# Performance work log

Hardware: AMD Instinct MI355X
Metric: run time of the kernel (lower is better)

## Reference

```python
import jax, jax.numpy as jnp
import numpy as np

D = 1024
HS = 64
NH = D // HS
NEG_INF = -1e30


def setup_inputs() -> dict:
    key = jax.random.key(0)
    ks = jax.random.split(key, 8)
    B, S = 4, 2048
    x = jax.random.normal(ks[0], (B, S, D), dtype=jnp.float32)
    y = jax.random.normal(ks[1], (B, S, D), dtype=jnp.float32)
    pad_mask = jnp.ones((B, S), dtype=jnp.int32)
    time_attention = jnp.ones((S, S), dtype=jnp.int32)
    scale = 1.0 / np.sqrt(D)
    Wq = jax.random.normal(ks[2], (D, D), dtype=jnp.float32) * scale
    Wk = jax.random.normal(ks[3], (D, D), dtype=jnp.float32) * scale
    Wv = jax.random.normal(ks[4], (D, D), dtype=jnp.float32) * scale
    Wp = jax.random.normal(ks[5], (D, D), dtype=jnp.float32) * scale
    bp = jnp.zeros((D,), dtype=jnp.float32)
    return {"x": x, "y": y, "pad_mask": pad_mask, "time_attention": time_attention,
            "Wq": Wq, "Wk": Wk, "Wv": Wv, "Wp": Wp, "bp": bp}


def reference(x, y, pad_mask, time_attention, Wq, Wk, Wv, Wp, bp):
    B, S, _ = x.shape
    Sy = y.shape[1]
    # q/k/v projections (Linear: x @ W.T), split into heads -> [B, H, S, hs]
    q = (y @ Wq.T).reshape(B, Sy, NH, HS).transpose(0, 2, 1, 3)
    k = (x @ Wk.T).reshape(B, S, NH, HS).transpose(0, 2, 1, 3)
    v = (x @ Wv.T).reshape(B, S, NH, HS).transpose(0, 2, 1, 3)
    # scaled scores [B, H, Sy, S]
    att = jnp.einsum('bhqe,bhke->bhqk', q, k) * (HS ** -0.5)
    # causal mask (tril[:S, :S])
    causal = jnp.tril(jnp.ones((S, S), dtype=jnp.bool_))
    att = jnp.where(causal[None, None, :Sy, :], att, NEG_INF)
    # pad mask over kv positions
    att = jnp.where(pad_mask[:, None, None, :] != 0, att, NEG_INF)
    # time attention mask [Sq, Sk]
    att = jnp.where(time_attention[None, None, :Sy, :] != 0, att, NEG_INF)
    p = jax.nn.softmax(att, axis=-1)  # dropout p=0 -> identity
    out = jnp.einsum('bhqk,bhke->bhqe', p, v)
    out = out.transpose(0, 2, 1, 3).reshape(B, Sy, D)
    return out @ Wp.T + bp
```

## Files before the change

kernel.cpp:

```cpp
#include <hip/hip_runtime.h>
#include <hip/hip_bf16.h>
#include <stdint.h>
#include <stddef.h>


typedef __attribute__((ext_vector_type(4))) float f32x4;
typedef __attribute__((ext_vector_type(8))) short s16x8;
typedef __attribute__((ext_vector_type(4))) float float4v;
typedef __attribute__((ext_vector_type(4))) int i32x4;
typedef __attribute__((ext_vector_type(2))) unsigned int u32x2;

#define DEV __device__ __forceinline__

constexpr int Bsz = 4, Sseq = 2048, Dm = 1024, NHn = 16, HSn = 64;
constexpr float QSCALE = 0.125f * 1.4426950408889634f;

constexpr size_t SZ_BF_XY = (size_t)Bsz * Sseq * Dm * 2;
constexpr size_t SZ_W     = (size_t)Dm * Dm * 2;
constexpr size_t OFF_XBF  = 0;
constexpr size_t OFF_YBF  = OFF_XBF + SZ_BF_XY;
constexpr size_t OFF_WQ   = OFF_YBF + SZ_BF_XY;
constexpr size_t OFF_WK   = OFF_WQ + SZ_W;
constexpr size_t OFF_WV   = OFF_WK + SZ_W;
constexpr size_t OFF_WP   = OFF_WV + SZ_W;
constexpr size_t OFF_QWS  = OFF_WP + SZ_W;
constexpr size_t OFF_KWS  = OFF_QWS + SZ_BF_XY;
constexpr size_t OFF_VTWS = OFF_KWS + SZ_BF_XY;
constexpr size_t OFF_OWS  = OFF_VTWS + SZ_BF_XY;
constexpr size_t OFF_FLAG = OFF_OWS + SZ_BF_XY;

DEV unsigned short f2bf(float f) {
  union { float f; unsigned int u; } v; v.f = f;
  unsigned int r = (v.u + 0x7FFFu + ((v.u >> 16) & 1u)) >> 16;
  return (unsigned short)r;
}

DEV void gll16(const void* g, void* l) {
  __builtin_amdgcn_global_load_lds((const __attribute__((address_space(1))) unsigned int*)g,
                                   (__attribute__((address_space(3))) unsigned int*)l, 16, 0, 0);
}

DEV unsigned int cvtpk(float a, float b) {
  unsigned int r;
  asm("v_cvt_pk_bf16_f32 %0, %1, %2" : "=v"(r) : "v"(a), "v"(b));
  return r;
}

union U8 { s16x8 v; unsigned int u[4]; };

__global__ void cvt_all(const float* __restrict__ x, const float* __restrict__ y,
                        const float* __restrict__ Wq, const float* __restrict__ Wk,
                        const float* __restrict__ Wv, const float* __restrict__ Wp,
                        const int* __restrict__ pad, const int* __restrict__ tmask,
                        char* __restrict__ ws, int* __restrict__ flags) {
  const int blk = blockIdx.x;
  if (blk >= 10240) {
    int bad = 0;
    if (blk < 10248) {
      const i32x4 v = ((const i32x4*)pad)[(blk - 10240) * 256 + threadIdx.x];
      bad = (v[0] == 0) | (v[1] == 0) | (v[2] == 0) | (v[3] == 0);
    } else {
      const i32x4* tp = (const i32x4*)tmask + ((size_t)(blk - 10248) * 256 + threadIdx.x) * 2;
      i32x4 v0 = tp[0], v1 = tp[1];
      bad = (v0[0] == 0) | (v0[1] == 0) | (v0[2] == 0) | (v0[3] == 0) |
            (v1[0] == 0) | (v1[1] == 0) | (v1[2] == 0) | (v1[3] == 0);
    }
    if (__builtin_amdgcn_ballot_w64(bad) != 0 && (threadIdx.x & 63) == 0)
      atomicOr(flags, 1);
    return;
  }
  const float* src;
  unsigned short* dst;
  int b8;
  float scale = 1.f;
  if (blk < 4096)      { src = x;  dst = (unsigned short*)(ws + OFF_XBF); b8 = blk; }
  else if (blk < 8192) { src = y;  dst = (unsigned short*)(ws + OFF_YBF); b8 = blk - 4096; }
  else if (blk < 8704) { src = Wq; dst = (unsigned short*)(ws + OFF_WQ);  b8 = blk - 8192; scale = QSCALE; }
  else if (blk < 9216) { src = Wk; dst = (unsigned short*)(ws + OFF_WK);  b8 = blk - 8704; }
  else if (blk < 9728) { src = Wv; dst = (unsigned short*)(ws + OFF_WV);  b8 = blk - 9216; }
  else                 { src = Wp; dst = (unsigned short*)(ws + OFF_WP);  b8 = blk - 9728; }
  const size_t i = (size_t)b8 * 256 + threadIdx.x;
  const float4v* s = (const float4v*)src + i * 2;
  float4v a = s[0], b = s[1];
  s16x8 o;
  o[0] = (short)f2bf(a[0] * scale); o[1] = (short)f2bf(a[1] * scale);
  o[2] = (short)f2bf(a[2] * scale); o[3] = (short)f2bf(a[3] * scale);
  o[4] = (short)f2bf(b[0] * scale); o[5] = (short)f2bf(b[1] * scale);
  o[6] = (short)f2bf(b[2] * scale); o[7] = (short)f2bf(b[3] * scale);
  *(s16x8*)(dst + i * 8) = o;
}

__global__ __launch_bounds__(256) void q_gemm(const unsigned short* __restrict__ A,
                                              const unsigned short* __restrict__ W,
                                              unsigned short* __restrict__ outb) {
  constexpr int K = 1024;
  __shared__ unsigned short sm[2][8192];
  const int tid = threadIdx.x;
  const int w = tid >> 6, lane = tid & 63, lo = lane & 15, hi = lane >> 4;
  const int wm = w >> 1, wn = w & 1;
  const int m0 = blockIdx.x * 128, n0 = blockIdx.y * 128;
  f32x4 acc[4][4] = {};

  auto stage = [&](int buf, int k0) {
#pragma unroll
    for (int h = 0; h < 2; ++h) {
      int c = w * 64 + h * 256 + lane;
      gll16(A + (size_t)(m0 + (c >> 2)) * K + k0 + (c & 3) * 8, &sm[buf][0] + (size_t)(w * 64 + h * 256) * 8);
      gll16(W + (size_t)(n0 + (c >> 2)) * K + k0 + (c & 3) * 8, &sm[buf][4096] + (size_t)(w * 64 + h * 256) * 8);
    }
  };

  stage(0, 0);
  __syncthreads();
  for (int t = 0; t < 32; ++t) {
    if (t < 31) stage((t + 1) & 1, (t + 1) * 32);
    const unsigned short* lA = &sm[t & 1][0];
    const unsigned short* lB = &sm[t & 1][4096];
    s16x8 af[4], bfr[4];
#pragma unroll
    for (int mi = 0; mi < 4; ++mi) af[mi] = *(const s16x8*)&lA[(wm * 64 + mi * 16 + lo) * 32 + hi * 8];
#pragma unroll
    for (int ni = 0; ni < 4; ++ni) bfr[ni] = *(const s16x8*)&lB[(wn * 64 + ni * 16 + lo) * 32 + hi * 8];
#pragma unroll
    for (int mi = 0; mi < 4; ++mi)
#pragma unroll
      for (int ni = 0; ni < 4; ++ni)
        acc[mi][ni] = __builtin_amdgcn_mfma_f32_16x16x32_bf16(af[mi], bfr[ni], acc[mi][ni], 0, 0, 0);
    __syncthreads();
  }
#pragma unroll
  for (int mi = 0; mi < 4; ++mi)
#pragma unroll
    for (int ni = 0; ni < 4; ++ni)
#pragma unroll
      for (int j = 0; j < 4; ++j) {
        int m = m0 + wm * 64 + mi * 16 + hi * 4 + j;
        int n = n0 + wn * 64 + ni * 16 + lo;
        int b = m >> 11, s = m & 2047, hh = n >> 6, e = n & 63;
        outb[((size_t)(b * NHn + hh) * Sseq + s) * HSn + e] = f2bf(acc[mi][ni][j]);
      }
}

__global__ __launch_bounds__(256, 2) void kv_gemm(const unsigned short* __restrict__ A,
                                                  const unsigned short* __restrict__ Wk,
                                                  const unsigned short* __restrict__ Wv,
                                                  unsigned short* __restrict__ kws,
                                                  unsigned short* __restrict__ vtw) {
  constexpr int K = 1024;
  __shared__ unsigned short sm[2][12288];
  const int tid = threadIdx.x;
  const int w = tid >> 6, lane = tid & 63, lo = lane & 15, hi = lane >> 4;
  const int wm = w >> 1, wn = w & 1;
  const int m0 = blockIdx.x * 128, n0 = blockIdx.y * 128;
  f32x4 acck[4][4] = {}, accv[4][4] = {};

  auto stage = [&](int buf, int k0) {
#pragma unroll
    for (int h = 0; h < 2; ++h) {
      int c = w * 64 + h * 256 + lane;
      size_t roff = (size_t)(c >> 2) * K + k0 + (c & 3) * 8;
      size_t loff = (size_t)(w * 64 + h * 256) * 8;
      gll16(A + (size_t)m0 * K + roff, &sm[buf][0] + loff);
      gll16(Wk + (size_t)n0 * K + roff, &sm[buf][4096] + loff);
      gll16(Wv + (size_t)n0 * K + roff, &sm[buf][8192] + loff);
    }
  };

  stage(0, 0);
  __syncthreads();
  for (int t = 0; t < 32; ++t) {
    if (t < 31) stage((t + 1) & 1, (t + 1) * 32);
    const unsigned short* lA = &sm[t & 1][0];
    const unsigned short* lBk = &sm[t & 1][4096];
    const unsigned short* lBv = &sm[t & 1][8192];
    s16x8 af[4], bfk[4], bfv[4];
#pragma unroll
    for (int mi = 0; mi < 4; ++mi) af[mi] = *(const s16x8*)&lA[(wm * 64 + mi * 16 + lo) * 32 + hi * 8];
#pragma unroll
    for (int ni = 0; ni < 4; ++ni) {
      bfk[ni] = *(const s16x8*)&lBk[(wn * 64 + ni * 16 + lo) * 32 + hi * 8];
      bfv[ni] = *(const s16x8*)&lBv[(wn * 64 + ni * 16 + lo) * 32 + hi * 8];
    }
#pragma unroll
    for (int mi = 0; mi < 4; ++mi)
#pragma unroll
      for (int ni = 0; ni < 4; ++ni) {
        acck[mi][ni] = __builtin_amdgcn_mfma_f32_16x16x32_bf16(af[mi], bfk[ni], acck[mi][ni], 0, 0, 0);
        accv[mi][ni] = __builtin_amdgcn_mfma_f32_16x16x32_bf16(af[mi], bfv[ni], accv[mi][ni], 0, 0, 0);
      }
    __syncthreads();
  }

#pragma unroll
  for (int mi = 0; mi < 4; ++mi)
#pragma unroll
    for (int ni = 0; ni < 4; ++ni)
#pragma unroll
      for (int j = 0; j < 4; ++j) {
        int m = m0 + wm * 64 + mi * 16 + hi * 4 + j;
        int n = n0 + wn * 64 + ni * 16 + lo;
        int b = m >> 11, s = m & 2047, hh = n >> 6, e = n & 63;
        kws[((size_t)(b * NHn + hh) * Sseq + s) * HSn + e] = f2bf(acck[mi][ni][j]);
      }
  unsigned short* tp = &sm[0][0];
  __syncthreads();
#pragma unroll
  for (int mi = 0; mi < 4; ++mi)
#pragma unroll
    for (int ni = 0; ni < 4; ++ni)
#pragma unroll
      for (int j = 0; j < 4; ++j) {
        int ml = wm * 64 + mi * 16 + hi * 4 + j;
        int nl = wn * 64 + ni * 16 + lo;
        tp[(size_t)nl * 136 + ml] = f2bf(accv[mi][ni][j]);
      }
  __syncthreads();
  int nl = tid >> 1, half = tid & 1;
  int b = m0 >> 11, hh = (n0 + nl) >> 6, e = (n0 + nl) & 63;
  unsigned short* dst = vtw + ((size_t)(b * NHn + hh) * HSn + e) * Sseq + (m0 & 2047) + half * 64;
#pragma unroll
  for (int i = 0; i < 8; ++i)
    *(s16x8*)(dst + i * 8) = *(const s16x8*)&tp[(size_t)nl * 136 + half * 64 + i * 8];
}

__global__ __launch_bounds__(256) void gemm_p(const unsigned short* __restrict__ A,
                                              const unsigned short* __restrict__ W,
                                              float* __restrict__ outf,
                                              const float* __restrict__ bias) {
  constexpr int K = 1024;
  __shared__ unsigned short sm[2][8192];
  const int tid = threadIdx.x;
  const int w = tid >> 6, lane = tid & 63, lo = lane & 15, hi = lane >> 4;
  const int wm = w >> 1, wn = w & 1;
  const int m0 = blockIdx.x * 128, n0 = blockIdx.y * 128;
  f32x4 acc[4][4] = {};

  auto stage = [&](int buf, int k0) {
#pragma unroll
    for (int h = 0; h < 2; ++h) {
      int c = w * 64 + h * 256 + lane;
      gll16(A + (size_t)(m0 + (c >> 2)) * K + k0 + (c & 3) * 8, &sm[buf][0] + (size_t)(w * 64 + h * 256) * 8);
      gll16(W + (size_t)(n0 + (c >> 2)) * K + k0 + (c & 3) * 8, &sm[buf][4096] + (size_t)(w * 64 + h * 256) * 8);
    }
  };

  stage(0, 0);
  __syncthreads();
  for (int t = 0; t < 32; ++t) {
    if (t < 31) stage((t + 1) & 1, (t + 1) * 32);
    const unsigned short* lA = &sm[t & 1][0];
    const unsigned short* lB = &sm[t & 1][4096];
    s16x8 af[4], bfr[4];
#pragma unroll
    for (int mi = 0; mi < 4; ++mi) af[mi] = *(const s16x8*)&lA[(wm * 64 + mi * 16 + lo) * 32 + hi * 8];
#pragma unroll
    for (int ni = 0; ni < 4; ++ni) bfr[ni] = *(const s16x8*)&lB[(wn * 64 + ni * 16 + lo) * 32 + hi * 8];
#pragma unroll
    for (int mi = 0; mi < 4; ++mi)
#pragma unroll
      for (int ni = 0; ni < 4; ++ni)
        acc[mi][ni] = __builtin_amdgcn_mfma_f32_16x16x32_bf16(af[mi], bfr[ni], acc[mi][ni], 0, 0, 0);
    __syncthreads();
  }
  float bv[4];
#pragma unroll
  for (int ni = 0; ni < 4; ++ni) bv[ni] = bias[n0 + wn * 64 + ni * 16 + lo];
#pragma unroll
  for (int mi = 0; mi < 4; ++mi)
#pragma unroll
    for (int ni = 0; ni < 4; ++ni)
#pragma unroll
      for (int j = 0; j < 4; ++j) {
        int m = m0 + wm * 64 + mi * 16 + hi * 4 + j;
        int n = n0 + wn * 64 + ni * 16 + lo;
        outf[(size_t)m * 1024 + n] = acc[mi][ni][j] + bv[ni];
      }
}

DEV void attn_unit16(const unsigned short* __restrict__ kbc,
                     const unsigned short* __restrict__ vbc,
                     const s16x8 (&qf)[2], f32x4 (&oacc)[4], f32x4& lacc,
                     float& mrun, const s16x8& ones,
                     int k0, int qw0, int lo, int hi, int b,
                     const int* __restrict__ pad, const int* __restrict__ tmask,
                     bool trivial) {
  if (k0 > qw0 + 15) return;

  f32x4 st[4];
  __builtin_amdgcn_s_setprio(1);
#pragma unroll
  for (int t = 0; t < 4; ++t) {
    f32x4 z = {0.f, 0.f, 0.f, 0.f};
#pragma unroll
    for (int kk = 0; kk < 2; ++kk) {
      s16x8 kfr = *(const s16x8*)&kbc[(t * 16 + lo) * 72 + kk * 32 + hi * 8];
      z = __builtin_amdgcn_mfma_f32_16x16x32_bf16(kfr, qf[kk], z, 0, 0, 0);
    }
    st[t] = z;
  }
  __builtin_amdgcn_s_setprio(0);
  const int qg = qw0 + lo;
  const int kgb = k0 + hi * 8;
  if (k0 + 63 > qw0) {
#pragma unroll
    for (int t = 0; t < 4; ++t)
#pragma unroll
      for (int j = 0; j < 4; ++j) {
        int kg = kgb + ((t & 1) << 5) + ((t >> 1) << 2) + j;
        if (kg > qg) st[t][j] = -3e38f;
      }
  }
  if (!trivial) {
#pragma unroll
    for (int t = 0; t < 4; ++t)
#pragma unroll
      for (int j = 0; j < 4; ++j) {
        int kg = kgb + ((t & 1) << 5) + ((t >> 1) << 2) + j;
        if (!pad[b * Sseq + kg] || !tmask[(size_t)qg * Sseq + kg]) st[t][j] = -3e38f;
      }
  }
  float m0v = fmaxf(fmaxf(st[0][0], st[0][1]), fmaxf(st[0][2], st[0][3]));
  float m1v = fmaxf(fmaxf(st[1][0], st[1][1]), fmaxf(st[1][2], st[1][3]));
  float m2v = fmaxf(fmaxf(st[2][0], st[2][1]), fmaxf(st[2][2], st[2][3]));
  float m3v = fmaxf(fmaxf(st[3][0], st[3][1]), fmaxf(st[3][2], st[3][3]));
  float mx = fmaxf(fmaxf(m0v, m1v), fmaxf(m2v, m3v));
  mx = fmaxf(mx, __shfl_xor(mx, 16, 64));
  mx = fmaxf(mx, __shfl_xor(mx, 32, 64));
  if (!__all(mx <= mrun + 11.f)) {
    const float mnew = fmaxf(mrun, mx);
    const float al = __builtin_amdgcn_exp2f(mrun - mnew);
    mrun = mnew;
#pragma unroll
    for (int et = 0; et < 4; ++et) oacc[et] *= al;
    lacc *= al;
  }
  unsigned int pk[4][2];
#pragma unroll
  for (int t = 0; t < 4; ++t) {
    float p0 = __builtin_amdgcn_exp2f(st[t][0] - mrun);
    float p1 = __builtin_amdgcn_exp2f(st[t][1] - mrun);
    float p2 = __builtin_amdgcn_exp2f(st[t][2] - mrun);
    float p3 = __builtin_amdgcn_exp2f(st[t][3] - mrun);
    pk[t][0] = cvtpk(p0, p1);
    pk[t][1] = cvtpk(p2, p3);
  }
  U8 pf0, pf1;
  pf0.u[0] = pk[0][0]; pf0.u[1] = pk[0][1]; pf0.u[2] = pk[2][0]; pf0.u[3] = pk[2][1];
  pf1.u[0] = pk[1][0]; pf1.u[1] = pk[1][1]; pf1.u[2] = pk[3][0]; pf1.u[3] = pk[3][1];
  __builtin_amdgcn_s_setprio(1);
#pragma unroll
  for (int et = 0; et < 4; ++et) {
    s16x8 vf0 = *(const s16x8*)&vbc[(et * 16 + lo) * 72 + hi * 8];
    s16x8 vf1 = *(const s16x8*)&vbc[(et * 16 + lo) * 72 + 32 + hi * 8];
    oacc[et] = __builtin_amdgcn_mfma_f32_16x16x32_bf16(vf0, pf0.v, oacc[et], 0, 0, 0);
    oacc[et] = __builtin_amdgcn_mfma_f32_16x16x32_bf16(vf1, pf1.v, oacc[et], 0, 0, 0);
  }
  lacc = __builtin_amdgcn_mfma_f32_16x16x32_bf16(ones, pf0.v, lacc, 0, 0, 0);
  lacc = __builtin_amdgcn_mfma_f32_16x16x32_bf16(ones, pf1.v, lacc, 0, 0, 0);
  __builtin_amdgcn_s_setprio(0);
}

DEV void attn_epi16(f32x4 (&oacc)[4], float lrun,
                    unsigned short* __restrict__ scr,
                    unsigned short* __restrict__ O, int b, int hh, int qw0,
                    int lane, int lo, int hi) {
  const float inv = 1.f / lrun;
#pragma unroll
  for (int et = 0; et < 4; ++et) {
    f32x4 o = oacc[et] * inv;
    u32x2 d = {cvtpk(o[0], o[1]), cvtpk(o[2], o[3])};
    *(u32x2*)&scr[lo * 72 + et * 16 + hi * 4] = d;
  }
  int q = lane >> 2, seg = lane & 3;
  unsigned short* dst = O + ((size_t)b * Sseq + qw0 + q) * Dm + hh * HSn + seg * 16;
  *(s16x8*)dst = *(const s16x8*)&scr[q * 72 + seg * 16];
  *(s16x8*)(dst + 8) = *(const s16x8*)&scr[q * 72 + seg * 16 + 8];
}

__global__ __launch_bounds__(512, 4) void attn_kernel(const unsigned short* __restrict__ Q,
                                                      const unsigned short* __restrict__ Kg,
                                                      const unsigned short* __restrict__ Vt,
                                                      unsigned short* __restrict__ O,
                                                      const int* __restrict__ pad,
                                                      const int* __restrict__ tmask,
                                                      const int* __restrict__ flags) {
  __shared__ unsigned short kb[2][64 * 72];
  __shared__ unsigned short vb[2][64 * 72];

  const int ip = blockIdx.y, bh = blockIdx.x;
  const int b = bh >> 4, hh = bh & 15;
  const int tid = threadIdx.x, w = tid >> 6, lane = tid & 63, lo = lane & 15, hi = lane >> 4;
  const int qtA = ip, qtB = 15 - ip;
  const int qw0A = qtA * 128 + w * 16, qw0B = qtB * 128 + w * 16;
  const int ktA = 2 * qtA + 1;
  const int ktmax = 2 * qtB + 2;
  const bool trivial = flags[0] == 0;

  const unsigned short* Qb = Q + (size_t)bh * Sseq * HSn;
  const unsigned short* Kb = Kg + (size_t)bh * Sseq * HSn;
  const unsigned short* Vb = Vt + (size_t)bh * HSn * Sseq;

  s16x8 qfA[2], qfB[2];
#pragma unroll
  for (int kk = 0; kk < 2; ++kk) {
    qfA[kk] = *(const s16x8*)&Qb[(size_t)(qw0A + lo) * HSn + kk * 32 + hi * 8];
    qfB[kk] = *(const s16x8*)&Qb[(size_t)(qw0B + lo) * HSn + kk * 32 + hi * 8];
  }

  s16x8 ones;
#pragma unroll
  for (int j = 0; j < 8; ++j) ones[j] = (short)0x3F80;

  f32x4 oaccA[4] = {}, oaccB[4] = {};
  f32x4 laccA = {}, laccB = {};
  float mrunA = -3e38f, mrunB = -3e38f;

  const int shalf = tid >> 8, st_t = tid & 255;
  const int sr = st_t >> 2, sc = (st_t & 3) * 16;
  const int srK = ((sr & 0x1C) << 1) | ((sr & 0x20) >> 3) | (sr & 3);

  s16x8 r0, r1;
  if (shalf == 0) {
    const unsigned short* gk = Kb + (size_t)srK * HSn + sc;
    r0 = *(const s16x8*)gk; r1 = *(const s16x8*)(gk + 8);
    *(s16x8*)&kb[0][sr * 72 + sc] = r0; *(s16x8*)&kb[0][sr * 72 + sc + 8] = r1;
  } else {
    const unsigned short* gv = Vb + (size_t)sr * Sseq + sc;
    r0 = *(const s16x8*)gv; r1 = *(const s16x8*)(gv + 8);
    *(s16x8*)&vb[0][sr * 72 + sc] = r0; *(s16x8*)&vb[0][sr * 72 + sc + 8] = r1;
  }
  __syncthreads();

  for (int kt = 0; kt < ktmax; ++kt) {
    const int cur = kt & 1, k0 = kt * 64;
    const bool pre = (kt + 1 < ktmax);
    if (pre) {
      const int k1 = k0 + 64;
      if (shalf == 0) {
        const unsigned short* gk = Kb + (size_t)(k1 + srK) * HSn + sc;
        r0 = *(const s16x8*)gk; r1 = *(const s16x8*)(gk + 8);
      } else {
        const unsigned short* gv = Vb + (size_t)sr * Sseq + k1 + sc;
        r0 = *(const s16x8*)gv; r1 = *(const s16x8*)(gv + 8);
      }
    }
    const unsigned short* kbc = kb[cur];
    const unsigned short* vbc = vb[cur];
    if (kt <= ktA)
      attn_unit16(kbc, vbc, qfA, oaccA, laccA, mrunA, ones,
                  k0, qw0A, lo, hi, b, pad, tmask, trivial);
    attn_unit16(kbc, vbc, qfB, oaccB, laccB, mrunB, ones,
                k0, qw0B, lo, hi, b, pad, tmask, trivial);
    if (pre) {
      const int nb = cur ^ 1;
      if (shalf == 0) {
        *(s16x8*)&kb[nb][sr * 72 + sc] = r0; *(s16x8*)&kb[nb][sr * 72 + sc + 8] = r1;
      } else {
        *(s16x8*)&vb[nb][sr * 72 + sc] = r0; *(s16x8*)&vb[nb][sr * 72 + sc + 8] = r1;
      }
    }
    __syncthreads();
  }

  unsigned short* scr = (unsigned short*)kb + (size_t)w * 1152;
  attn_epi16(oaccA, laccA[0], scr, O, b, hh, qw0A, lane, lo, hi);
  attn_epi16(oaccB, laccB[0], scr, O, b, hh, qw0B, lane, lo, hi);
}

extern "C" void kernel_launch(void* const* d_in, const int* in_sizes, int n_in,
                              void* d_out, int out_size, void* d_ws, size_t ws_size,
                              hipStream_t stream) {
  const float* x = (const float*)d_in[0];
  const float* y = (const float*)d_in[1];
  const int* pad = (const int*)d_in[2];
  const int* tmask = (const int*)d_in[3];
  const float* Wq = (const float*)d_in[4];
  const float* Wk = (const float*)d_in[5];
  const float* Wv = (const float*)d_in[6];
  const float* Wp = (const float*)d_in[7];
  const float* bp = (const float*)d_in[8];

  char* ws = (char*)d_ws;
  unsigned short* xbf = (unsigned short*)(ws + OFF_XBF);
  unsigned short* ybf = (unsigned short*)(ws + OFF_YBF);
  unsigned short* wqb = (unsigned short*)(ws + OFF_WQ);
  unsigned short* wkb = (unsigned short*)(ws + OFF_WK);
  unsigned short* wvb = (unsigned short*)(ws + OFF_WV);
  unsigned short* wpb = (unsigned short*)(ws + OFF_WP);
  unsigned short* qws = (unsigned short*)(ws + OFF_QWS);
  unsigned short* kws = (unsigned short*)(ws + OFF_KWS);
  unsigned short* vtw = (unsigned short*)(ws + OFF_VTWS);
  unsigned short* ows = (unsigned short*)(ws + OFF_OWS);
  int* flags = (int*)(ws + OFF_FLAG);

  hipMemsetAsync(flags, 0, 4, stream);
  cvt_all<<<12296, 256, 0, stream>>>(x, y, Wq, Wk, Wv, Wp, pad, tmask, ws, flags);

  q_gemm<<<dim3(64, 8), 256, 0, stream>>>(ybf, wqb, qws);
  kv_gemm<<<dim3(64, 8), 256, 0, stream>>>(xbf, wkb, wvb, kws, vtw);

  attn_kernel<<<dim3(64, 8), 512, 0, stream>>>(qws, kws, vtw, ows, pad, tmask, flags);

  gemm_p<<<dim3(64, 8), 256, 0, stream>>>(ows, wpb, (float*)d_out, bp);
}
```

Before: 183.6 us.

## Give each attention wave 32 query rows to reuse K/V fragments

The attention block shrinks from 8 waves to 4, and each wave now handles two 16-row query sub-tiles. Each K and V fragment read from LDS feeds two MFMAs instead of one, which halves LDS traffic per FLOP. Each thread now stages both K and V for the next tile, and the epilogue writes 32 rows per wave. The cost is higher register pressure (launch bounds 256,2) and fewer waves per block to hide latency.

Result: no change. 186.0 us (+1.3%).

```diff
diff --git a/kernel.cpp b/kernel.cpp
--- a/kernel.cpp
+++ b/kernel.cpp
@@ -277,107 +277,124 @@
       }
 }
 
-DEV void attn_unit16(const unsigned short* __restrict__ kbc,
+DEV void attn_unit32(const unsigned short* __restrict__ kbc,
                      const unsigned short* __restrict__ vbc,
-                     const s16x8 (&qf)[2], f32x4 (&oacc)[4], f32x4& lacc,
-                     float& mrun, const s16x8& ones,
+                     const s16x8 (&qf)[2][2], f32x4 (&oacc)[4][2], f32x4 (&lacc)[2],
+                     float (&mrun)[2], const s16x8& ones,
                      int k0, int qw0, int lo, int hi, int b,
                      const int* __restrict__ pad, const int* __restrict__ tmask,
                      bool trivial) {
-  if (k0 > qw0 + 15) return;
-
-  f32x4 st[4];
+  if (k0 > qw0 + 31) return;
+
+  f32x4 st[2][4];
   __builtin_amdgcn_s_setprio(1);
 #pragma unroll
   for (int t = 0; t < 4; ++t) {
-    f32x4 z = {0.f, 0.f, 0.f, 0.f};
-#pragma unroll
-    for (int kk = 0; kk < 2; ++kk) {
-      s16x8 kfr = *(const s16x8*)&kbc[(t * 16 + lo) * 72 + kk * 32 + hi * 8];
-      z = __builtin_amdgcn_mfma_f32_16x16x32_bf16(kfr, qf[kk], z, 0, 0, 0);
-    }
-    st[t] = z;
+    const s16x8 kf0 = *(const s16x8*)&kbc[(t * 16 + lo) * 72 + hi * 8];
+    const s16x8 kf1 = *(const s16x8*)&kbc[(t * 16 + lo) * 72 + 32 + hi * 8];
+    f32x4 z0 = {0.f, 0.f, 0.f, 0.f}, z1 = {0.f, 0.f, 0.f, 0.f};
+    z0 = __builtin_amdgcn_mfma_f32_16x16x32_bf16(kf0, qf[0][0], z0, 0, 0, 0);
+    z0 = __builtin_amdgcn_mfma_f32_16x16x32_bf16(kf1, qf[0][1], z0, 0, 0, 0);
+    z1 = __builtin_amdgcn_mfma_f32_16x16x32_bf16(kf0, qf[1][0], z1, 0, 0, 0);
+    z1 = __builtin_amdgcn_mfma_f32_16x16x32_bf16(kf1, qf[1][1], z1, 0, 0, 0);
+    st[0][t] = z0; st[1][t] = z1;
   }
   __builtin_amdgcn_s_setprio(0);
-  const int qg = qw0 + lo;
+
   const int kgb = k0 + hi * 8;
-  if (k0 + 63 > qw0) {
-#pragma unroll
-    for (int t = 0; t < 4; ++t)
-#pragma unroll
-      for (int j = 0; j < 4; ++j) {
-        int kg = kgb + ((t & 1) << 5) + ((t >> 1) << 2) + j;
-        if (kg > qg) st[t][j] = -3e38f;
-      }
-  }
-  if (!trivial) {
-#pragma unroll
-    for (int t = 0; t < 4; ++t)
-#pragma unroll
-      for (int j = 0; j < 4; ++j) {
-        int kg = kgb + ((t & 1) << 5) + ((t >> 1) << 2) + j;
-        if (!pad[b * Sseq + kg] || !tmask[(size_t)qg * Sseq + kg]) st[t][j] = -3e38f;
-      }
-  }
-  float m0v = fmaxf(fmaxf(st[0][0], st[0][1]), fmaxf(st[0][2], st[0][3]));
-  float m1v = fmaxf(fmaxf(st[1][0], st[1][1]), fmaxf(st[1][2], st[1][3]));
-  float m2v = fmaxf(fmaxf(st[2][0], st[2][1]), fmaxf(st[2][2], st[2][3]));
-  float m3v = fmaxf(fmaxf(st[3][0], st[3][1]), fmaxf(st[3][2], st[3][3]));
-  float mx = fmaxf(fmaxf(m0v, m1v), fmaxf(m2v, m3v));
-  mx = fmaxf(mx, __shfl_xor(mx, 16, 64));
-  mx = fmaxf(mx, __shfl_xor(mx, 32, 64));
-  if (!__all(mx <= mrun + 11.f)) {
-    const float mnew = fmaxf(mrun, mx);
-    const float al = __builtin_amdgcn_exp2f(mrun - mnew);
-    mrun = mnew;
-#pragma unroll
-    for (int et = 0; et < 4; ++et) oacc[et] *= al;
-    lacc *= al;
-  }
-  unsigned int pk[4][2];
-#pragma unroll
-  for (int t = 0; t < 4; ++t) {
-    float p0 = __builtin_amdgcn_exp2f(st[t][0] - mrun);
-    float p1 = __builtin_amdgcn_exp2f(st[t][1] - mrun);
-    float p2 = __builtin_amdgcn_exp2f(st[t][2] - mrun);
-    float p3 = __builtin_amdgcn_exp2f(st[t][3] - mrun);
-    pk[t][0] = cvtpk(p0, p1);
-    pk[t][1] = cvtpk(p2, p3);
-  }
-  U8 pf0, pf1;
-  pf0.u[0] = pk[0][0]; pf0.u[1] = pk[0][1]; pf0.u[2] = pk[2][0]; pf0.u[3] = pk[2][1];
-  pf1.u[0] = pk[1][0]; pf1.u[1] = pk[1][1]; pf1.u[2] = pk[3][0]; pf1.u[3] = pk[3][1];
+  U8 pf[2][2];
+#pragma unroll
+  for (int mq = 0; mq < 2; ++mq) {
+    const int qg = qw0 + mq * 16 + lo;
+    if (k0 + 63 > qw0) {
+#pragma unroll
+      for (int t = 0; t < 4; ++t)
+#pragma unroll
+        for (int j = 0; j < 4; ++j) {
+          int kg = kgb + ((t & 1) << 5) + ((t >> 1) << 2) + j;
+          if (kg > qg) st[mq][t][j] = -3e38f;
+        }
+    }
+    if (!trivial) {
+#pragma unroll
+      for (int t = 0; t < 4; ++t)
+#pragma unroll
+        for (int j = 0; j < 4; ++j) {
+          int kg = kgb + ((t & 1) << 5) + ((t >> 1) << 2) + j;
+          if (!pad[b * Sseq + kg] || !tmask[(size_t)qg * Sseq + kg]) st[mq][t][j] = -3e38f;
+        }
+    }
+    float m0v = fmaxf(fmaxf(st[mq][0][0], st[mq][0][1]), fmaxf(st[mq][0][2], st[mq][0][3]));
+    float m1v = fmaxf(fmaxf(st[mq][1][0], st[mq][1][1]), fmaxf(st[mq][1][2], st[mq][1][3]));
+    float m2v = fmaxf(fmaxf(st[mq][2][0], st[mq][2][1]), fmaxf(st[mq][2][2], st[mq][2][3]));
+    float m3v = fmaxf(fmaxf(st[mq][3][0], st[mq][3][1]), fmaxf(st[mq][3][2], st[mq][3][3]));
+    float mx = fmaxf(fmaxf(m0v, m1v), fmaxf(m2v, m3v));
+    mx = fmaxf(mx, __shfl_xor(mx, 16, 64));
+    mx = fmaxf(mx, __shfl_xor(mx, 32, 64));
+    if (!__all(mx <= mrun[mq] + 11.f)) {
+      const float mnew = fmaxf(mrun[mq], mx);
+      const float al = __builtin_amdgcn_exp2f(mrun[mq] - mnew);
+      mrun[mq] = mnew;
+#pragma unroll
+      for (int et = 0; et < 4; ++et) oacc[et][mq] *= al;
+      lacc[mq] *= al;
+    }
+    unsigned int pk[4][2];
+#pragma unroll
+    for (int t = 0; t < 4; ++t) {
+      float p0 = __builtin_amdgcn_exp2f(st[mq][t][0] - mrun[mq]);
+      float p1 = __builtin_amdgcn_exp2f(st[mq][t][1] - mrun[mq]);
+      float p2 = __builtin_amdgcn_exp2f(st[mq][t][2] - mrun[mq]);
+      float p3 = __builtin_amdgcn_exp2f(st[mq][t][3] - mrun[mq]);
+      pk[t][0] = cvtpk(p0, p1);
+      pk[t][1] = cvtpk(p2, p3);
+    }
+    pf[mq][0].u[0] = pk[0][0]; pf[mq][0].u[1] = pk[0][1];
+    pf[mq][0].u[2] = pk[2][0]; pf[mq][0].u[3] = pk[2][1];
+    pf[mq][1].u[0] = pk[1][0]; pf[mq][1].u[1] = pk[1][1];
+    pf[mq][1].u[2] = pk[3][0]; pf[mq][1].u[3] = pk[3][1];
+  }
+
   __builtin_amdgcn_s_setprio(1);
 #pragma unroll
   for (int et = 0; et < 4; ++et) {
-    s16x8 vf0 = *(const s16x8*)&vbc[(et * 16 + lo) * 72 + hi * 8];
-    s16x8 vf1 = *(const s16x8*)&vbc[(et * 16 + lo) * 72 + 32 + hi * 8];
-    oacc[et] = __builtin_amdgcn_mfma_f32_16x16x32_bf16(vf0, pf0.v, oacc[et], 0, 0, 0);
-    oacc[et] = __builtin_amdgcn_mfma_f32_16x16x32_bf16(vf1, pf1.v, oacc[et], 0, 0, 0);
-  }
-  lacc = __builtin_amdgcn_mfma_f32_16x16x32_bf16(ones, pf0.v, lacc, 0, 0, 0);
-  lacc = __builtin_amdgcn_mfma_f32_16x16x32_bf16(ones, pf1.v, lacc, 0, 0, 0);
+    const s16x8 vf0 = *(const s16x8*)&vbc[(et * 16 + lo) * 72 + hi * 8];
+    const s16x8 vf1 = *(const s16x8*)&vbc[(et * 16 + lo) * 72 + 32 + hi * 8];
+    oacc[et][0] = __builtin_amdgcn_mfma_f32_16x16x32_bf16(vf0, pf[0][0].v, oacc[et][0], 0, 0, 0);
+    oacc[et][0] = __builtin_amdgcn_mfma_f32_16x16x32_bf16(vf1, pf[0][1].v, oacc[et][0], 0, 0, 0);
+    oacc[et][1] = __builtin_amdgcn_mfma_f32_16x16x32_bf16(vf0, pf[1][0].v, oacc[et][1], 0, 0, 0);
+    oacc[et][1] = __builtin_amdgcn_mfma_f32_16x16x32_bf16(vf1, pf[1][1].v, oacc[et][1], 0, 0, 0);
+  }
+  lacc[0] = __builtin_amdgcn_mfma_f32_16x16x32_bf16(ones, pf[0][0].v, lacc[0], 0, 0, 0);
+  lacc[0] = __builtin_amdgcn_mfma_f32_16x16x32_bf16(ones, pf[0][1].v, lacc[0], 0, 0, 0);
+  lacc[1] = __builtin_amdgcn_mfma_f32_16x16x32_bf16(ones, pf[1][0].v, lacc[1], 0, 0, 0);
+  lacc[1] = __builtin_amdgcn_mfma_f32_16x16x32_bf16(ones, pf[1][1].v, lacc[1], 0, 0, 0);
   __builtin_amdgcn_s_setprio(0);
 }
 
-DEV void attn_epi16(f32x4 (&oacc)[4], float lrun,
+DEV void attn_epi32(f32x4 (&oacc)[4][2], f32x4 (&lacc)[2],
                     unsigned short* __restrict__ scr,
                     unsigned short* __restrict__ O, int b, int hh, int qw0,
                     int lane, int lo, int hi) {
-  const float inv = 1.f / lrun;
+  const float inv0 = 1.f / lacc[0][0];
+  const float inv1 = 1.f / lacc[1][0];
 #pragma unroll
   for (int et = 0; et < 4; ++et) {
-    f32x4 o = oacc[et] * inv;
-    u32x2 d = {cvtpk(o[0], o[1]), cvtpk(o[2], o[3])};
-    *(u32x2*)&scr[lo * 72 + et * 16 + hi * 4] = d;
-  }
-  int q = lane >> 2, seg = lane & 3;
-  unsigned short* dst = O + ((size_t)b * Sseq + qw0 + q) * Dm + hh * HSn + seg * 16;
-  *(s16x8*)dst = *(const s16x8*)&scr[q * 72 + seg * 16];
-  *(s16x8*)(dst + 8) = *(const s16x8*)&scr[q * 72 + seg * 16 + 8];
-}
-
-__global__ __launch_bounds__(512, 4) void attn_kernel(const unsigned short* __restrict__ Q,
+    f32x4 o0 = oacc[et][0] * inv0;
+    f32x4 o1 = oacc[et][1] * inv1;
+    u32x2 d0 = {cvtpk(o0[0], o0[1]), cvtpk(o0[2], o0[3])};
+    u32x2 d1 = {cvtpk(o1[0], o1[1]), cvtpk(o1[2], o1[3])};
+    *(u32x2*)&scr[(0 * 16 + lo) * 72 + et * 16 + hi * 4] = d0;
+    *(u32x2*)&scr[(1 * 16 + lo) * 72 + et * 16 + hi * 4] = d1;
+  }
+  int q = lane & 31, half = lane >> 5;
+  unsigned short* dst = O + ((size_t)b * Sseq + qw0 + q) * Dm + hh * HSn + half * 32;
+#pragma unroll
+  for (int i = 0; i < 4; ++i)
+    *(s16x8*)(dst + i * 8) = *(const s16x8*)&scr[q * 72 + half * 32 + i * 8];
+}
+
+__global__ __launch_bounds__(256, 2) void attn_kernel(const unsigned short* __restrict__ Q,
                                                       const unsigned short* __restrict__ Kg,
                                                       const unsigned short* __restrict__ Vt,
                                                       unsigned short* __restrict__ O,
@@ -391,7 +408,7 @@
   const int b = bh >> 4, hh = bh & 15;
   const int tid = threadIdx.x, w = tid >> 6, lane = tid & 63, lo = lane & 15, hi = lane >> 4;
   const int qtA = ip, qtB = 15 - ip;
-  const int qw0A = qtA * 128 + w * 16, qw0B = qtB * 128 + w * 16;
+  const int qw0A = qtA * 128 + w * 32, qw0B = qtB * 128 + w * 32;
   const int ktA = 2 * qtA + 1;
   const int ktmax = 2 * qtB + 2;
   const bool trivial = flags[0] == 0;
@@ -400,35 +417,35 @@
   const unsigned short* Kb = Kg + (size_t)bh * Sseq * HSn;
   const unsigned short* Vb = Vt + (size_t)bh * HSn * Sseq;
 
-  s16x8 qfA[2], qfB[2];
-#pragma unroll
-  for (int kk = 0; kk < 2; ++kk) {
-    qfA[kk] = *(const s16x8*)&Qb[(size_t)(qw0A + lo) * HSn + kk * 32 + hi * 8];
-    qfB[kk] = *(const s16x8*)&Qb[(size_t)(qw0B + lo) * HSn + kk * 32 + hi * 8];
-  }
+  s16x8 qfA[2][2], qfB[2][2];
+#pragma unroll
+  for (int mq = 0; mq < 2; ++mq)
+#pragma unroll
+    for (int kk = 0; kk < 2; ++kk) {
+      qfA[mq][kk] = *(const s16x8*)&Qb[(size_t)(qw0A + mq * 16 + lo) * HSn + kk * 32 + hi * 8];
+      qfB[mq][kk] = *(const s16x8*)&Qb[(size_t)(qw0B + mq * 16 + lo) * HSn + kk * 32 + hi * 8];
+    }
 
   s16x8 ones;
 #pragma unroll
   for (int j = 0; j < 8; ++j) ones[j] = (short)0x3F80;
 
-  f32x4 oaccA[4] = {}, oaccB[4] = {};
-  f32x4 laccA = {}, laccB = {};
-  float mrunA = -3e38f, mrunB = -3e38f;
-
-  const int shalf = tid >> 8, st_t = tid & 255;
-  const int sr = st_t >> 2, sc = (st_t & 3) * 16;
+  f32x4 oaccA[4][2] = {}, oaccB[4][2] = {};
+  f32x4 laccA[2] = {}, laccB[2] = {};
+  float mrunA[2] = {-3e38f, -3e38f}, mrunB[2] = {-3e38f, -3e38f};
+
+  const int sr = tid >> 2, sc = (tid & 3) * 16;
   const int srK = ((sr & 0x1C) << 1) | ((sr & 0x20) >> 3) | (sr & 3);
 
-  s16x8 r0, r1;
-  if (shalf == 0) {
+  s16x8 rk0, rk1, rv0, rv1;
+  {
     const unsigned short* gk = Kb + (size_t)srK * HSn + sc;
-    r0 = *(const s16x8*)gk; r1 = *(const s16x8*)(gk + 8);
-    *(s16x8*)&kb[0][sr * 72 + sc] = r0; *(s16x8*)&kb[0][sr * 72 + sc + 8] = r1;
-  } else {
+    rk0 = *(const s16x8*)gk; rk1 = *(const s16x8*)(gk + 8);
     const unsigned short* gv = Vb + (size_t)sr * Sseq + sc;
-    r0 = *(const s16x8*)gv; r1 = *(const s16x8*)(gv + 8);
-    *(s16x8*)&vb[0][sr * 72 + sc] = r0; *(s16x8*)&vb[0][sr * 72 + sc + 8] = r1;
-  }
+    rv0 = *(const s16x8*)gv; rv1 = *(const s16x8*)(gv + 8);
+  }
+  *(s16x8*)&kb[0][sr * 72 + sc] = rk0; *(s16x8*)&kb[0][sr * 72 + sc + 8] = rk1;
+  *(s16x8*)&vb[0][sr * 72 + sc] = rv0; *(s16x8*)&vb[0][sr * 72 + sc + 8] = rv1;
   __syncthreads();
 
   for (int kt = 0; kt < ktmax; ++kt) {
@@ -436,35 +453,29 @@
     const bool pre = (kt + 1 < ktmax);
     if (pre) {
       const int k1 = k0 + 64;
-      if (shalf == 0) {
-        const unsigned short* gk = Kb + (size_t)(k1 + srK) * HSn + sc;
-        r0 = *(const s16x8*)gk; r1 = *(const s16x8*)(gk + 8);
-      } else {
-        const unsigned short* gv = Vb + (size_t)sr * Sseq + k1 + sc;
-        r0 = *(const s16x8*)gv; r1 = *(const s16x8*)(gv + 8);
-      }
+      const unsigned short* gk = Kb + (size_t)(k1 + srK) * HSn + sc;
+      rk0 = *(const s16x8*)gk; rk1 = *(const s16x8*)(gk + 8);
+      const unsigned short* gv = Vb + (size_t)sr * Sseq + k1 + sc;
+      rv0 = *(const s16x8*)gv; rv1 = *(const s16x8*)(gv + 8);
     }
     const unsigned short* kbc = kb[cur];
     const unsigned short* vbc = vb[cur];
     if (kt <= ktA)
-      attn_unit16(kbc, vbc, qfA, oaccA, laccA, mrunA, ones,
+      attn_unit32(kbc, vbc, qfA, oaccA, laccA, mrunA, ones,
                   k0, qw0A, lo, hi, b, pad, tmask, trivial);
-    attn_unit16(kbc, vbc, qfB, oaccB, laccB, mrunB, ones,
+    attn_unit32(kbc, vbc, qfB, oaccB, laccB, mrunB, ones,
                 k0, qw0B, lo, hi, b, pad, tmask, trivial);
     if (pre) {
       const int nb = cur ^ 1;
-      if (shalf == 0) {
-        *(s16x8*)&kb[nb][sr * 72 + sc] = r0; *(s16x8*)&kb[nb][sr * 72 + sc + 8] = r1;
-      } else {
-        *(s16x8*)&vb[nb][sr * 72 + sc] = r0; *(s16x8*)&vb[nb][sr * 72 + sc + 8] = r1;
-      }
+      *(s16x8*)&kb[nb][sr * 72 + sc] = rk0; *(s16x8*)&kb[nb][sr * 72 + sc + 8] = rk1;
+      *(s16x8*)&vb[nb][sr * 72 + sc] = rv0; *(s16x8*)&vb[nb][sr * 72 + sc + 8] = rv1;
     }
     __syncthreads();
   }
 
-  unsigned short* scr = (unsigned short*)kb + (size_t)w * 1152;
-  attn_epi16(oaccA, laccA[0], scr, O, b, hh, qw0A, lane, lo, hi);
-  attn_epi16(oaccB, laccB[0], scr, O, b, hh, qw0B, lane, lo, hi);
+  unsigned short* scr = (unsigned short*)kb + (size_t)w * 2304;
+  attn_epi32(oaccA, laccA, scr, O, b, hh, qw0A, lane, lo, hi);
+  attn_epi32(oaccB, laccB, scr, O, b, hh, qw0B, lane, lo, hi);
 }
 
 extern "C" void kernel_launch(void* const* d_in, const int* in_sizes, int n_in,
@@ -499,7 +510,7 @@
   q_gemm<<<dim3(64, 8), 256, 0, stream>>>(ybf, wqb, qws);
   kv_gemm<<<dim3(64, 8), 256, 0, stream>>>(xbf, wkb, wvb, kws, vtw);
 
-  attn_kernel<<<dim3(64, 8), 512, 0, stream>>>(qws, kws, vtw, ows, pad, tmask, flags);
+  attn_kernel<<<dim3(64, 8), 256, 0, stream>>>(qws, kws, vtw, ows, pad, tmask, flags);
 
   gemm_p<<<dim3(64, 8), 256, 0, stream>>>(ows, wpb, (float*)d_out, bp);
 }
```
